# Kernel optimization log

Measured on AMD Instinct MI355X. Metric: run time of the kernel, lower is better.

Reference implementation:

```python
import jax, jax.numpy as jnp
import numpy as np

B, IN, O, K = 2048, 8192, 4096, 64


def setup_inputs() -> dict:
    key = jax.random.key(0)
    k1, k2, k3 = jax.random.split(key, 3)
    x = jax.random.normal(k1, (B, IN), dtype=jnp.float32)
    indices = jax.random.randint(k2, (O, K), 0, IN, dtype=jnp.int32)
    weight = jax.random.normal(k3, (O, K), dtype=jnp.float32) * 0.1
    bias = jnp.zeros((O,), dtype=jnp.float32)
    return {"x": x, "indices": indices, "weight": weight, "bias": bias}


def reference(x, indices, weight, bias):
    # Gather K selected input features per output unit: [B, O, K]
    x_sel = jnp.take(x, indices, axis=1)
    # Weighted reduce over K, add bias: [B, O]
    out = jnp.einsum('bok,ok->bo', x_sel, weight) + bias
    return out
```

## Files before the change

### kernel.cpp

```cpp
#include <hip/hip_runtime.h>
#include <cstdint>
#include <cstddef>

#define B_ 2048
#define IN_ 8192
#define O_ 4096
#define K_ 64
#define BP_ (B_ / 2)

typedef float vfloat4 __attribute__((ext_vector_type(4)));

__device__ __forceinline__ float blo(uint32_t p) { return __uint_as_float(p << 16); }
__device__ __forceinline__ float bhi(uint32_t p) { return __uint_as_float(p & 0xffff0000u); }

__global__ __launch_bounds__(256) void xpose_pack(const float* __restrict__ x,
                                                  uint32_t* __restrict__ xT) {
    __shared__ uint16_t T[64][65];
    const int t  = threadIdx.x;
    const int b0 = blockIdx.x << 6;
    const int i0 = blockIdx.y << 6;
    const int il = t & 63;
    const int bq = t >> 6;
#pragma unroll
    for (int r = 0; r < 16; ++r) {
        int bl = (bq << 4) + r;
        float v = x[(size_t)(b0 + bl) * IN_ + i0 + il];
        uint32_t u = __float_as_uint(v);
        u += 0x7fffu + ((u >> 16) & 1u);
        T[il][bl] = (uint16_t)(u >> 16);
    }
    __syncthreads();
#pragma unroll
    for (int r = 0; r < 8; ++r) {
        int flat = t + (r << 8);
        int iw = flat >> 5;
        int bp = flat & 31;
        uint32_t lo = T[iw][2 * bp];
        uint32_t hi = T[iw][2 * bp + 1];
        __builtin_nontemporal_store(lo | (hi << 16),
                                    &xT[(size_t)(i0 + iw) * BP_ + (b0 >> 1) + bp]);
    }
}

__global__ __launch_bounds__(256, 8) void spl_main(const uint32_t* __restrict__ xT,
                                                   const int* __restrict__ idx,
                                                   const float* __restrict__ w,
                                                   const float* __restrict__ bias,
                                                   float* __restrict__ out) {
    __shared__ float tile[256][17];
    const int t     = threadIdx.x;
    const int lane  = t & 63;
    const int f     = blockIdx.x;
    const int btile = f & 7;
    const int otile = f >> 3;
    const int obase = otile << 4;
    const int bbase = btile << 8;
    const int cv    = 2 * lane;
    const int cbase = bbase >> 1;
    const int wv    = __builtin_amdgcn_readfirstlane(t >> 6);

    for (int oi = 0; oi < 4; ++oi) {
        const int o = obase + (wv << 2) + oi;
        const int*   ip = idx + o * K_;
        const float* wp = w + o * K_;
        float a0 = 0.f, a1 = 0.f, a2 = 0.f, a3 = 0.f;
#pragma unroll
        for (int kb = 0; kb < 4; ++kb) {
            uint2 q[16];
#pragma unroll
            for (int j = 0; j < 16; ++j) {
                int row = ip[(kb << 4) + j];
                q[j] = *(const uint2*)(xT + ((size_t)row << 10) + cbase + cv);
            }
            __builtin_amdgcn_sched_barrier(0);
#pragma unroll
            for (int j = 0; j < 16; ++j) {
                float wj = wp[(kb << 4) + j];
                a0 = fmaf(blo(q[j].x), wj, a0);
                a1 = fmaf(bhi(q[j].x), wj, a1);
                a2 = fmaf(blo(q[j].y), wj, a2);
                a3 = fmaf(bhi(q[j].y), wj, a3);
            }
        }
        const float bo = bias[o];
        const int ol = (wv << 2) + oi;
        const int bl0 = 4 * lane;
        tile[bl0 + 0][ol] = a0 + bo;
        tile[bl0 + 1][ol] = a1 + bo;
        tile[bl0 + 2][ol] = a2 + bo;
        tile[bl0 + 3][ol] = a3 + bo;
    }
    __syncthreads();
    const int bl_ = t >> 2;
    const int ol4 = (t & 3) << 2;
#pragma unroll
    for (int r = 0; r < 4; ++r) {
        int bl = bl_ + (r << 6);
        vfloat4 v;
        v.x = tile[bl][ol4 + 0];
        v.y = tile[bl][ol4 + 1];
        v.z = tile[bl][ol4 + 2];
        v.w = tile[bl][ol4 + 3];
        __builtin_nontemporal_store(v,
            (vfloat4*)&out[(size_t)(bbase + bl) * O_ + obase + ol4]);
    }
}

__global__ __launch_bounds__(256) void spl_naive(const float* __restrict__ x,
                                                 const int* __restrict__ idx,
                                                 const float* __restrict__ w,
                                                 const float* __restrict__ bias,
                                                 float* __restrict__ out) {
    int o = blockIdx.x * 256 + threadIdx.x;
    int b = blockIdx.y;
    const float* xr = x + (size_t)b * IN_;
    float acc = bias[o];
    for (int k = 0; k < K_; ++k)
        acc = fmaf(xr[idx[o * K_ + k]], w[o * K_ + k], acc);
    out[(size_t)b * O_ + o] = acc;
}

extern "C" void kernel_launch(void* const* d_in, const int* in_sizes, int n_in,
                              void* d_out, int out_size, void* d_ws, size_t ws_size,
                              hipStream_t stream) {
    const float* x    = (const float*)d_in[0];
    const int*   idx  = (const int*)d_in[1];
    const float* w    = (const float*)d_in[2];
    const float* bias = (const float*)d_in[3];
    float*       out  = (float*)d_out;

    const size_t xt_bytes = (size_t)IN_ * BP_ * sizeof(uint32_t);
    if (ws_size >= xt_bytes) {
        uint32_t* xT = (uint32_t*)d_ws;
        hipLaunchKernelGGL(xpose_pack, dim3(B_ / 64, IN_ / 64), dim3(256), 0, stream, x, xT);
        hipLaunchKernelGGL(spl_main, dim3((O_ / 16) * (B_ / 256)), dim3(256), 0, stream,
                           xT, idx, w, bias, out);
    } else {
        hipLaunchKernelGGL(spl_naive, dim3(O_ / 256, B_), dim3(256), 0, stream,
                           x, idx, w, bias, out);
    }
}
```

Measured before the change: 89.66 us.

## Stage gathered xT rows through LDS with double-buffered global_load_lds pipeline

Replaces the direct per-lane 8-byte gathers from the transposed bf16 x with 16-byte global_load_lds transfers into a per-wave double-buffered LDS stage. The next 8 indices are prefetched while the current 8 are read back with inline ds_read_b64 and consumed. The aim is wider, fully coalesced global requests and overlap of gather latency with the FMAs. In exchange it uses 32KB more LDS per block and lowers the occupancy hint from 8 to 4 blocks per CU. It also relies on manual vmcnt/lgkmcnt waits and hand-computed LDS offsets, which are fragile and could be wrong.

```diff
diff --git a/kernel.cpp b/kernel.cpp
--- a/kernel.cpp
+++ b/kernel.cpp
@@ -9,9 +9,19 @@
 #define BP_ (B_ / 2)
 
 typedef float vfloat4 __attribute__((ext_vector_type(4)));
+typedef uint32_t v2u  __attribute__((ext_vector_type(2)));
 
 __device__ __forceinline__ float blo(uint32_t p) { return __uint_as_float(p << 16); }
 __device__ __forceinline__ float bhi(uint32_t p) { return __uint_as_float(p & 0xffff0000u); }
+
+__device__ __forceinline__ void stage16(const uint32_t* g, uint32_t* l) {
+    __builtin_amdgcn_global_load_lds(
+        (const __attribute__((address_space(1))) void*)g,
+        (__attribute__((address_space(3))) void*)l, 16, 0, 0);
+}
+
+#define DSR(dst, OFF) asm volatile("ds_read_b64 %0, %1 offset:" #OFF \
+                                   : "=v"(dst) : "v"(va))
 
 __global__ __launch_bounds__(256) void xpose_pack(const float* __restrict__ x,
                                                   uint32_t* __restrict__ xT) {
@@ -42,45 +52,84 @@
     }
 }
 
-__global__ __launch_bounds__(256, 8) void spl_main(const uint32_t* __restrict__ xT,
+__global__ __launch_bounds__(256, 4) void spl_main(const uint32_t* __restrict__ xT,
                                                    const int* __restrict__ idx,
                                                    const float* __restrict__ w,
                                                    const float* __restrict__ bias,
                                                    float* __restrict__ out) {
     __shared__ float tile[256][17];
+    __shared__ uint32_t stage[4][2048];
     const int t     = threadIdx.x;
     const int lane  = t & 63;
+    const int half  = lane >> 5;
+    const int l5    = lane & 31;
     const int f     = blockIdx.x;
     const int btile = f & 7;
     const int otile = f >> 3;
     const int obase = otile << 4;
     const int bbase = btile << 8;
-    const int cv    = 2 * lane;
     const int cbase = bbase >> 1;
     const int wv    = __builtin_amdgcn_readfirstlane(t >> 6);
+    uint32_t* const sw = &stage[wv][0];
+
+    typedef __attribute__((address_space(3))) uint32_t lds_u32;
+    const uint32_t va = (uint32_t)(size_t)(lds_u32*)sw + ((uint32_t)lane << 3);
 
     for (int oi = 0; oi < 4; ++oi) {
         const int o = obase + (wv << 2) + oi;
         const int*   ip = idx + o * K_;
         const float* wp = w + o * K_;
         float a0 = 0.f, a1 = 0.f, a2 = 0.f, a3 = 0.f;
+
 #pragma unroll
-        for (int kb = 0; kb < 4; ++kb) {
-            uint2 q[16];
+        for (int j = 0; j < 4; ++j) {
+            int r0 = ip[2 * j];
+            int r1 = ip[2 * j + 1];
+            const uint32_t* src = xT + ((size_t)(half ? r1 : r0) << 10)
+                                     + cbase + (l5 << 2);
+            stage16(src, sw + j * 256);
+        }
 #pragma unroll
-            for (int j = 0; j < 16; ++j) {
-                int row = ip[(kb << 4) + j];
-                q[j] = *(const uint2*)(xT + ((size_t)row << 10) + cbase + cv);
+        for (int tb = 0; tb < 8; ++tb) {
+            if (tb < 7) {
+                const int nb = tb + 1;
+                uint32_t* dst = sw + (nb & 1) * 1024;
+#pragma unroll
+                for (int j = 0; j < 4; ++j) {
+                    int k2 = (nb << 3) + 2 * j;
+                    int r0 = ip[k2];
+                    int r1 = ip[k2 + 1];
+                    const uint32_t* src = xT + ((size_t)(half ? r1 : r0) << 10)
+                                             + cbase + (l5 << 2);
+                    stage16(src, dst + j * 256);
+                }
+                asm volatile("s_waitcnt vmcnt(4)" ::: "memory");
+            } else {
+                asm volatile("s_waitcnt vmcnt(0)" ::: "memory");
             }
             __builtin_amdgcn_sched_barrier(0);
-#pragma unroll
-            for (int j = 0; j < 16; ++j) {
-                float wj = wp[(kb << 4) + j];
-                a0 = fmaf(blo(q[j].x), wj, a0);
-                a1 = fmaf(bhi(q[j].x), wj, a1);
-                a2 = fmaf(blo(q[j].y), wj, a2);
-                a3 = fmaf(bhi(q[j].y), wj, a3);
+            v2u q0, q1, q2, q3, q4, q5, q6, q7;
+            if ((tb & 1) == 0) {
+                DSR(q0, 0);    DSR(q1, 512);  DSR(q2, 1024); DSR(q3, 1536);
+                DSR(q4, 2048); DSR(q5, 2560); DSR(q6, 3072); DSR(q7, 3584);
+            } else {
+                DSR(q0, 4096); DSR(q1, 4608); DSR(q2, 5120); DSR(q3, 5632);
+                DSR(q4, 6144); DSR(q5, 6656); DSR(q6, 7168); DSR(q7, 7680);
             }
+            asm volatile("s_waitcnt lgkmcnt(0)" ::: "memory");
+            __builtin_amdgcn_sched_barrier(0);
+#define CONS(Q, S)                                                  \
+            {                                                       \
+                float wj = wp[(tb << 3) + (S)];                     \
+                a0 = fmaf(blo(Q.x), wj, a0);                        \
+                a1 = fmaf(bhi(Q.x), wj, a1);                        \
+                a2 = fmaf(blo(Q.y), wj, a2);                        \
+                a3 = fmaf(bhi(Q.y), wj, a3);                        \
+            }
+            CONS(q0, 0) CONS(q1, 1) CONS(q2, 2) CONS(q3, 3)
+            CONS(q4, 4) CONS(q5, 5) CONS(q6, 6) CONS(q7, 7)
+#undef CONS
+            __builtin_amdgcn_sched_barrier(0);
         }
         const float bo = bias[o];
         const int ol = (wv << 2) + oi;
```

Measured after the change: 86.65 us. -3.4%, faster.
